# Optimization experiments

Measured on AMD Instinct MI355X. Metric: run time of the kernel, lower is better.

## Reference

```python
import jax, jax.numpy as jnp
import numpy as np

N_NODES = 100000
IN_C, HID_C, OUT_C = 128, 64, 5
NEG_SLOPE = 0.01  # F.leaky_relu default


def gcn_conv(x, W, b, src_sl, dst_sl, norm, n_nodes):
    """PyG GCNConv: h = D^{-1/2}(A+I)D^{-1/2} (x W) + b.
    src_sl/dst_sl already include self-loops; norm is the per-edge coefficient."""
    h = x @ W                              # [N, out]
    msg = h[src_sl] * norm[:, None]        # [E+N, out] gather + scale
    agg = jax.ops.segment_sum(msg, dst_sl, num_segments=n_nodes)
    return agg + b


def setup_inputs() -> dict:
    key = jax.random.key(0)
    ks = jax.random.split(key, 8)
    n, e = N_NODES, 1600000
    x = jax.random.normal(ks[0], (n, IN_C), dtype=jnp.float32)
    edge_index = jax.random.randint(ks[1], (2, e), 0, n, dtype=jnp.int64)
    idx = jax.random.randint(ks[2], (20000,), 0, n, dtype=jnp.int64)
    # Glorot-ish init for GCNConv weights, kaiming-ish for MLP
    W0 = jax.random.normal(ks[3], (IN_C, HID_C), dtype=jnp.float32) * (1.0 / np.sqrt(IN_C))
    b0 = jnp.zeros((HID_C,), dtype=jnp.float32)
    W1 = jax.random.normal(ks[4], (HID_C, HID_C), dtype=jnp.float32) * (1.0 / np.sqrt(HID_C))
    b1 = jnp.zeros((HID_C,), dtype=jnp.float32)
    Wm = jax.random.normal(ks[5], (HID_C, OUT_C), dtype=jnp.float32) * (1.0 / np.sqrt(HID_C))
    bm = jnp.zeros((OUT_C,), dtype=jnp.float32)
    return {"x": x, "edge_index": edge_index, "idx": idx,
            "W0": W0, "b0": b0, "W1": W1, "b1": b1, "Wm": Wm, "bm": bm}


def reference(x, edge_index, idx, W0, b0, W1, b1, Wm, bm):
    n = x.shape[0]
    src, dst = edge_index[0], edge_index[1]
    loops = jnp.arange(n, dtype=edge_index.dtype)
    src_sl = jnp.concatenate([src, loops])
    dst_sl = jnp.concatenate([dst, loops])
    # symmetric normalization with self-loops (gcn_norm)
    deg = jax.ops.segment_sum(jnp.ones_like(dst_sl, dtype=x.dtype), dst_sl, num_segments=n)
    dinv = jnp.where(deg > 0, jax.lax.rsqrt(deg), 0.0)
    norm = dinv[src_sl] * dinv[dst_sl]     # [E+N]

    h = jax.nn.leaky_relu(gcn_conv(x, W0, b0, src_sl, dst_sl, norm, n), NEG_SLOPE)
    h = jax.nn.leaky_relu(gcn_conv(h, W1, b1, src_sl, dst_sl, norm, n), NEG_SLOPE)

    h_sel = h[idx]                          # index_select on node dim
    out = jax.nn.sigmoid(h_sel @ Wm + bm)
    return (h_sel, out)
```

## Files before the change

### kernel.cpp

```cpp
#include <hip/hip_runtime.h>
#include <hip/hip_fp16.h>
#include <math.h>


#define NPART 256
#define MAXB 2048

typedef _Float16 h8 __attribute__((ext_vector_type(8)));
typedef float f4v __attribute__((ext_vector_type(4)));

__device__ __forceinline__ float lrelu(float x) { return x > 0.0f ? x : 0.01f * x; }


__global__ __launch_bounds__(1024) void k_part_hist(const int* __restrict__ dst, int E,
                                                    int B, int* __restrict__ phist) {
    __shared__ int scnt[MAXB];
    int t = threadIdx.x, p = blockIdx.x;
    for (int i = t; i < B; i += 1024) scnt[i] = 0;
    __syncthreads();
    int ep = (((E + NPART - 1) / NPART) + 3) & ~3;
    int beg = p * ep, endi = min(E, beg + ep);
    int cnt4 = (endi - beg) >> 2;
    for (int i = t; i < cnt4; i += 1024) {
        int4 d = *(const int4*)(dst + beg + i * 4);
        atomicAdd(&scnt[d.x >> 6], 1);
        atomicAdd(&scnt[d.y >> 6], 1);
        atomicAdd(&scnt[d.z >> 6], 1);
        atomicAdd(&scnt[d.w >> 6], 1);
    }
    int rem = (endi - beg) & 3;
    if (t < rem) atomicAdd(&scnt[dst[beg + cnt4 * 4 + t] >> 6], 1);
    __syncthreads();
    for (int i = t; i < B; i += 1024) phist[i * NPART + p] = scnt[i];
}

__global__ __launch_bounds__(1024) void k_part_scatter(const int* __restrict__ src,
                                                       const int* __restrict__ dst, int E,
                                                       int B, const int* __restrict__ pbase,
                                                       int* __restrict__ esA) {
    __shared__ int sbase[MAXB];
    int t = threadIdx.x, p = blockIdx.x;
    for (int i = t; i < B; i += 1024) sbase[i] = pbase[i * NPART + p];
    __syncthreads();
    int ep = (((E + NPART - 1) / NPART) + 3) & ~3;
    int beg = p * ep, endi = min(E, beg + ep);
    int cnt4 = (endi - beg) >> 2;
    for (int i = t; i < cnt4; i += 1024) {
        int e = beg + i * 4;
        int4 d = *(const int4*)(dst + e);
        int4 s = *(const int4*)(src + e);
        int p0 = atomicAdd(&sbase[d.x >> 6], 1);
        int p1 = atomicAdd(&sbase[d.y >> 6], 1);
        int p2 = atomicAdd(&sbase[d.z >> 6], 1);
        int p3 = atomicAdd(&sbase[d.w >> 6], 1);
        esA[p0] = ((d.x & 63) << 24) | s.x;
        esA[p1] = ((d.y & 63) << 24) | s.y;
        esA[p2] = ((d.z & 63) << 24) | s.z;
        esA[p3] = ((d.w & 63) << 24) | s.w;
    }
    int rem = (endi - beg) & 3;
    if (t < rem) {
        int e = beg + cnt4 * 4 + t;
        int d = dst[e];
        int pos = atomicAdd(&sbase[d >> 6], 1);
        esA[pos] = ((d & 63) << 24) | src[e];
    }
}


__global__ void k_blocksum(const int* __restrict__ cnt, int N, int* __restrict__ bsum) {
    __shared__ int sm[256];
    int b = blockIdx.x, t = threadIdx.x;
    int base = b * 1024 + t * 4;
    int s = 0;
#pragma unroll
    for (int i = 0; i < 4; ++i) { int j = base + i; if (j < N) s += cnt[j]; }
    sm[t] = s; __syncthreads();
    for (int off = 128; off > 0; off >>= 1) {
        if (t < off) sm[t] += sm[t + off];
        __syncthreads();
    }
    if (t == 0) bsum[b] = sm[0];
}

__global__ void k_scan_bsum(int* __restrict__ bsum, int nb, int* __restrict__ offN) {
    __shared__ int sm[1024];
    int t = threadIdx.x;
    int v = (t < nb) ? bsum[t] : 0;
    sm[t] = v; __syncthreads();
    for (int d = 1; d < 1024; d <<= 1) {
        int add = (t >= d) ? sm[t - d] : 0;
        __syncthreads();
        sm[t] += add;
        __syncthreads();
    }
    if (t < nb) bsum[t] = sm[t] - v;
    if (t == nb - 1) *offN = sm[t];
}

__global__ void k_scan_block(const int* __restrict__ cnt, const int* __restrict__ bsum,
                             int* __restrict__ off, int N) {
    __shared__ int sm[256];
    int b = blockIdx.x, t = threadIdx.x;
    int base = b * 1024 + t * 4;
    int v[4];
#pragma unroll
    for (int i = 0; i < 4; ++i) { int j = base + i; v[i] = (j < N) ? cnt[j] : 0; }
    int tsum = v[0] + v[1] + v[2] + v[3];
    sm[t] = tsum; __syncthreads();
    for (int d = 1; d < 256; d <<= 1) {
        int val = (t >= d) ? sm[t - d] : 0;
        __syncthreads();
        sm[t] += val;
        __syncthreads();
    }
    int run = sm[t] - tsum + bsum[b];
#pragma unroll
    for (int i = 0; i < 4; ++i) {
        int j = base + i;
        if (j < N) off[j] = run;
        run += v[i];
    }
}


__global__ __launch_bounds__(256) void k_bsort(const int* __restrict__ pbase, int BP,
                                               const int* __restrict__ esA,
                                               int* __restrict__ esB,
                                               int* __restrict__ off,
                                               float* __restrict__ dinv,
                                               int N, int E) {
    __shared__ int hcnt[64];
    __shared__ int hoff[64];
    int t = threadIdx.x, b = blockIdx.x;
    int start = pbase[b * NPART];
    int endi  = pbase[min((b + 1) * NPART, BP)];
    int cnt = endi - start;

    if (t < 64) hcnt[t] = 0;
    __syncthreads();
    for (int i = t * 4; i < cnt; i += 1024) {
#pragma unroll
        for (int c = 0; c < 4; ++c)
            if (i + c < cnt) atomicAdd(&hcnt[(esA[start + i + c] >> 24) & 63], 1);
    }
    __syncthreads();

    if (t < 64) {
        int c = hcnt[t];
        int v = c;
#pragma unroll
        for (int d = 1; d < 64; d <<= 1) {
            int u = __shfl_up(v, d);
            if (t >= d) v += u;
        }
        int pos = start + (v - c);
        hoff[t] = pos;
        int g = b * 64 + t;
        if (g < N) {
            off[g] = pos;
            dinv[g] = rsqrtf((float)c + 1.0f);
        }
        if (g == N - 1) off[N] = E;
    }
    __syncthreads();
    if (t < 64) hcnt[t] = hoff[t];
    __syncthreads();

    for (int i = t * 4; i < cnt; i += 1024) {
#pragma unroll
        for (int c = 0; c < 4; ++c)
            if (i + c < cnt) {
                int v = esA[start + i + c];
                int pos = atomicAdd(&hcnt[(v >> 24) & 63], 1);
                esB[pos] = v & 0xFFFFFF;
            }
    }
}


template <int K, typename AT>
__global__ __launch_bounds__(256) void k_gemm(const AT* __restrict__ A,
                                              const float* __restrict__ W,
                                              const float* __restrict__ dinv,
                                              __half* __restrict__ hout, int N) {
    constexpr int ASTR = K + 8;
    __shared__ _Float16 a16[64 * ASTR];
    __shared__ _Float16 wt16[64 * ASTR];
    int t = threadIdx.x, lane = t & 63, wv = t >> 6;
    int rowBase = blockIdx.x * 64;

#pragma unroll
    for (int i = 0; i < K / 16; ++i) {
        int g = i * 256 + t;
        int r = g / (K / 4), kq = g % (K / 4);
        int gr = rowBase + r; if (gr >= N) gr = N - 1;
        _Float16* p = a16 + r * ASTR + kq * 4;
        if constexpr (sizeof(AT) == 4) {
            float4 v = *(const float4*)((const float*)A + (size_t)gr * K + kq * 4);
            *(__half2*)(p)     = __floats2half2_rn(v.x, v.y);
            *(__half2*)(p + 2) = __floats2half2_rn(v.z, v.w);
        } else {
            *(uint2*)p = *(const uint2*)((const __half*)A + (size_t)gr * K + kq * 4);
        }
    }
#pragma unroll
    for (int i = 0; i < K / 16; ++i) {
        int g = i * 256 + t;
        int k = g >> 4, nq = g & 15;
        float4 v = *(const float4*)(W + (size_t)k * 64 + nq * 4);
        wt16[(nq * 4 + 0) * ASTR + k] = (_Float16)v.x;
        wt16[(nq * 4 + 1) * ASTR + k] = (_Float16)v.y;
        wt16[(nq * 4 + 2) * ASTR + k] = (_Float16)v.z;
        wt16[(nq * 4 + 3) * ASTR + k] = (_Float16)v.w;
    }
    __syncthreads();

    int m = lane & 15, q = lane >> 4;
    f4v acc[4] = {{0,0,0,0},{0,0,0,0},{0,0,0,0},{0,0,0,0}};
    const _Float16* arow = a16 + (wv * 16 + m) * ASTR + q * 8;
#pragma unroll
    for (int kt = 0; kt < K / 32; ++kt) {
        h8 af = *(const h8*)(arow + kt * 32);
#pragma unroll
        for (int nt = 0; nt < 4; ++nt) {
            h8 bf = *(const h8*)(wt16 + (nt * 16 + m) * ASTR + kt * 32 + q * 8);
            acc[nt] = __builtin_amdgcn_mfma_f32_16x16x32_f16(af, bf, acc[nt], 0, 0, 0);
        }
    }

    int r0 = rowBase + wv * 16 + q * 4;
#pragma unroll
    for (int reg = 0; reg < 4; ++reg) {
        int row = r0 + reg;
        if (row >= N) continue;
        float dv = dinv[row];
#pragma unroll
        for (int nt = 0; nt < 4; ++nt)
            hout[(size_t)row * 64 + nt * 16 + m] = (__half)(acc[nt][reg] * dv);
    }
}


__global__ __launch_bounds__(256) void k_agg1(const int* __restrict__ off,
                                              const int* __restrict__ esB,
                                              const float* __restrict__ dinv,
                                              const __half* __restrict__ hs,
                                              const float* __restrict__ b0,
                                              __half* __restrict__ aout, int N) {
    int lane = threadIdx.x & 63;
    int node = (blockIdx.x * blockDim.x + threadIdx.x) >> 6;
    if (node >= N) return;
    int qt = lane >> 4, l16 = lane & 15;
    int beg = off[node], end = off[node + 1];
    float dv = dinv[node];
    float4 b = *(const float4*)(b0 + l16 * 4);

    float ax = 0, ay = 0, az = 0, aw = 0;
    auto ld = [&](int s) { return *(const uint2*)(hs + (size_t)s * 64 + l16 * 4); };
    auto acc4 = [&](uint2 u) {
        float2 f0 = __half22float2(*(__half2*)&u.x);
        float2 f1 = __half22float2(*(__half2*)&u.y);
        ax += f0.x; ay += f0.y; az += f1.x; aw += f1.y;
    };
    if (qt == 0) acc4(ld(node));

    for (int base = beg; base < end; base += 64) {
        int nb = min(end - base, 64);
        int myIdx = esB[min(base + lane, end - 1)];
        if (nb <= 16) {
            int s0 = __shfl(myIdx, min(qt,      nb - 1));
            int s1 = __shfl(myIdx, min(qt + 4,  nb - 1));
            int s2 = __shfl(myIdx, min(qt + 8,  nb - 1));
            int s3 = __shfl(myIdx, min(qt + 12, nb - 1));
            uint2 u0 = ld(s0), u1 = ld(s1), u2 = ld(s2), u3 = ld(s3);
            if (qt      < nb) acc4(u0);
            if (qt + 4  < nb) acc4(u1);
            if (qt + 8  < nb) acc4(u2);
            if (qt + 12 < nb) acc4(u3);
        } else {
            int s0 = __shfl(myIdx, min(qt,      nb - 1));
            int s1 = __shfl(myIdx, min(qt + 4,  nb - 1));
            int s2 = __shfl(myIdx, min(qt + 8,  nb - 1));
            int s3 = __shfl(myIdx, min(qt + 12, nb - 1));
            int s4 = __shfl(myIdx, min(qt + 16, nb - 1));
            int s5 = __shfl(myIdx, min(qt + 20, nb - 1));
            int s6 = __shfl(myIdx, min(qt + 24, nb - 1));
            int s7 = __shfl(myIdx, min(qt + 28, nb - 1));
            uint2 u0 = ld(s0), u1 = ld(s1), u2 = ld(s2), u3 = ld(s3);
            uint2 u4 = ld(s4), u5 = ld(s5), u6 = ld(s6), u7 = ld(s7);
            acc4(u0);
            if (qt + 4  < nb) acc4(u1);
            if (qt + 8  < nb) acc4(u2);
            if (qt + 12 < nb) acc4(u3);
            if (qt + 16 < nb) acc4(u4);
            if (qt + 20 < nb) acc4(u5);
            if (qt + 24 < nb) acc4(u6);
            if (qt + 28 < nb) acc4(u7);
            if (nb > 32) {
                int t0 = __shfl(myIdx, min(qt + 32, nb - 1));
                int t1 = __shfl(myIdx, min(qt + 36, nb - 1));
                int t2 = __shfl(myIdx, min(qt + 40, nb - 1));
                int t3 = __shfl(myIdx, min(qt + 44, nb - 1));
                int t4 = __shfl(myIdx, min(qt + 48, nb - 1));
                int t5 = __shfl(myIdx, min(qt + 52, nb - 1));
                int t6 = __shfl(myIdx, min(qt + 56, nb - 1));
                int t7 = __shfl(myIdx, min(qt + 60, nb - 1));
                uint2 v0 = ld(t0), v1 = ld(t1), v2 = ld(t2), v3 = ld(t3);
                uint2 v4 = ld(t4), v5 = ld(t5), v6 = ld(t6), v7 = ld(t7);
                if (qt + 32 < nb) acc4(v0);
                if (qt + 36 < nb) acc4(v1);
                if (qt + 40 < nb) acc4(v2);
                if (qt + 44 < nb) acc4(v3);
                if (qt + 48 < nb) acc4(v4);
                if (qt + 52 < nb) acc4(v5);
                if (qt + 56 < nb) acc4(v6);
                if (qt + 60 < nb) acc4(v7);
            }
        }
    }

#pragma unroll
    for (int d = 16; d <= 32; d <<= 1) {
        ax += __shfl_xor(ax, d); ay += __shfl_xor(ay, d);
        az += __shfl_xor(az, d); aw += __shfl_xor(aw, d);
    }
    if (qt == 0) {
        float ox = lrelu(ax * dv + b.x), oy = lrelu(ay * dv + b.y);
        float oz = lrelu(az * dv + b.z), ow = lrelu(aw * dv + b.w);
        uint2 u;
        *(__half2*)&u.x = __floats2half2_rn(ox, oy);
        *(__half2*)&u.y = __floats2half2_rn(oz, ow);
        *(uint2*)(aout + (size_t)node * 64 + l16 * 4) = u;
    }
}


__global__ __launch_bounds__(256) void k_aggout(const int* __restrict__ idx,
                                                const int* __restrict__ off,
                                                const int* __restrict__ esB,
                                                const float* __restrict__ dinv,
                                                const __half* __restrict__ hs,
                                                const float* __restrict__ b1,
                                                const float* __restrict__ Wm,
                                                const float* __restrict__ bm,
                                                float* __restrict__ out, int NSEL) {
    int lane = threadIdx.x & 63;
    int wv = (blockIdx.x * blockDim.x + threadIdx.x) >> 6;
    if (wv >= NSEL) return;
    int node = idx[wv];
    int qt = lane >> 4, l16 = lane & 15;
    int beg = off[node], end = off[node + 1];
    float dv = dinv[node];
    float4 b = *(const float4*)(b1 + l16 * 4);

    float ax = 0, ay = 0, az = 0, aw = 0;
    auto ld = [&](int s) { return *(const uint2*)(hs + (size_t)s * 64 + l16 * 4); };
    auto acc4 = [&](uint2 u) {
        float2 f0 = __half22float2(*(__half2*)&u.x);
        float2 f1 = __half22float2(*(__half2*)&u.y);
        ax += f0.x; ay += f0.y; az += f1.x; aw += f1.y;
    };
    if (qt == 0) acc4(ld(node));

    for (int base = beg; base < end; base += 64) {
        int nb = min(end - base, 64);
        int myIdx = esB[min(base + lane, end - 1)];
        if (nb <= 16) {
            int s0 = __shfl(myIdx, min(qt,      nb - 1));
            int s1 = __shfl(myIdx, min(qt + 4,  nb - 1));
            int s2 = __shfl(myIdx, min(qt + 8,  nb - 1));
            int s3 = __shfl(myIdx, min(qt + 12, nb - 1));
            uint2 u0 = ld(s0), u1 = ld(s1), u2 = ld(s2), u3 = ld(s3);
            if (qt      < nb) acc4(u0);
            if (qt + 4  < nb) acc4(u1);
            if (qt + 8  < nb) acc4(u2);
            if (qt + 12 < nb) acc4(u3);
        } else {
            int s0 = __shfl(myIdx, min(qt,      nb - 1));
            int s1 = __shfl(myIdx, min(qt + 4,  nb - 1));
            int s2 = __shfl(myIdx, min(qt + 8,  nb - 1));
            int s3 = __shfl(myIdx, min(qt + 12, nb - 1));
            int s4 = __shfl(myIdx, min(qt + 16, nb - 1));
            int s5 = __shfl(myIdx, min(qt + 20, nb - 1));
            int s6 = __shfl(myIdx, min(qt + 24, nb - 1));
            int s7 = __shfl(myIdx, min(qt + 28, nb - 1));
            uint2 u0 = ld(s0), u1 = ld(s1), u2 = ld(s2), u3 = ld(s3);
            uint2 u4 = ld(s4), u5 = ld(s5), u6 = ld(s6), u7 = ld(s7);
            acc4(u0);
            if (qt + 4  < nb) acc4(u1);
            if (qt + 8  < nb) acc4(u2);
            if (qt + 12 < nb) acc4(u3);
            if (qt + 16 < nb) acc4(u4);
            if (qt + 20 < nb) acc4(u5);
            if (qt + 24 < nb) acc4(u6);
            if (qt + 28 < nb) acc4(u7);
            if (nb > 32) {
                int t0 = __shfl(myIdx, min(qt + 32, nb - 1));
                int t1 = __shfl(myIdx, min(qt + 36, nb - 1));
                int t2 = __shfl(myIdx, min(qt + 40, nb - 1));
                int t3 = __shfl(myIdx, min(qt + 44, nb - 1));
                int t4 = __shfl(myIdx, min(qt + 48, nb - 1));
                int t5 = __shfl(myIdx, min(qt + 52, nb - 1));
                int t6 = __shfl(myIdx, min(qt + 56, nb - 1));
                int t7 = __shfl(myIdx, min(qt + 60, nb - 1));
                uint2 v0 = ld(t0), v1 = ld(t1), v2 = ld(t2), v3 = ld(t3);
                uint2 v4 = ld(t4), v5 = ld(t5), v6 = ld(t6), v7 = ld(t7);
                if (qt + 32 < nb) acc4(v0);
                if (qt + 36 < nb) acc4(v1);
                if (qt + 40 < nb) acc4(v2);
                if (qt + 44 < nb) acc4(v3);
                if (qt + 48 < nb) acc4(v4);
                if (qt + 52 < nb) acc4(v5);
                if (qt + 56 < nb) acc4(v6);
                if (qt + 60 < nb) acc4(v7);
            }
        }
    }

#pragma unroll
    for (int d = 16; d <= 32; d <<= 1) {
        ax += __shfl_xor(ax, d); ay += __shfl_xor(ay, d);
        az += __shfl_xor(az, d); aw += __shfl_xor(aw, d);
    }

    float4 hsel;
    hsel.x = lrelu(ax * dv + b.x); hsel.y = lrelu(ay * dv + b.y);
    hsel.z = lrelu(az * dv + b.z); hsel.w = lrelu(aw * dv + b.w);
    if (qt == 0) *(float4*)(out + (size_t)wv * 64 + l16 * 4) = hsel;

    const float* wr = Wm + (size_t)(4 * l16) * 5;
#pragma unroll
    for (int o = 0; o < 5; ++o) {
        float p = hsel.x * wr[o] + hsel.y * wr[5 + o] +
                  hsel.z * wr[10 + o] + hsel.w * wr[15 + o];
        p += __shfl_xor(p, 1); p += __shfl_xor(p, 2);
        p += __shfl_xor(p, 4); p += __shfl_xor(p, 8);
        if (lane == 0)
            out[(size_t)NSEL * 64 + (size_t)wv * 5 + o] =
                1.0f / (1.0f + expf(-(p + bm[o])));
    }
}

extern "C" void kernel_launch(void* const* d_in, const int* in_sizes, int n_in,
                              void* d_out, int out_size, void* d_ws, size_t ws_size,
                              hipStream_t stream) {
    const float* x   = (const float*)d_in[0];
    const int*   ei  = (const int*)d_in[1];
    const int*   idx = (const int*)d_in[2];
    const float* W0  = (const float*)d_in[3];
    const float* b0  = (const float*)d_in[4];
    const float* W1  = (const float*)d_in[5];
    const float* b1  = (const float*)d_in[6];
    const float* Wm  = (const float*)d_in[7];
    const float* bm  = (const float*)d_in[8];

    int N    = in_sizes[0] / 128;
    int E    = in_sizes[1] / 2;
    int NSEL = in_sizes[2];
    const int* src = ei;
    const int* dst = ei + E;

    int B  = (N + 63) / 64;
    int BP = B * NPART;

    char* w = (char*)d_ws;
    size_t Na  = ((size_t)N + 1023) & ~(size_t)1023;
    size_t Ea  = ((size_t)E + 1023) & ~(size_t)1023;
    size_t BPa = ((size_t)BP + 1023) & ~(size_t)1023;
    float*  dinv  = (float*)w;                w += Na * 4;
    int*    phist = (int*)w;                  w += BPa * 4;
    int*    pbase = (int*)w;                  w += (BPa + 1024) * 4;
    int*    bsum  = (int*)w;                  w += 1024 * 4;
    int*    off   = (int*)w;                  w += (Na + 1024) * 4;
    int*    esA   = (int*)w;                  w += Ea * 4;
    int*    esB   = (int*)w;                  w += Ea * 4;
    __half* hs16  = (__half*)w;               w += (size_t)N * 64 * 2;
    __half* a16g  = (__half*)w;

    int nbp = (BP + 1023) / 1024;

    k_part_hist<<<NPART, 1024, 0, stream>>>(dst, E, B, phist);
    k_blocksum<<<nbp, 256, 0, stream>>>(phist, BP, bsum);
    k_scan_bsum<<<1, 1024, 0, stream>>>(bsum, nbp, pbase + BP);
    k_scan_block<<<nbp, 256, 0, stream>>>(phist, bsum, pbase, BP);
    k_part_scatter<<<NPART, 1024, 0, stream>>>(src, dst, E, B, pbase, esA);
    k_bsort<<<B, 256, 0, stream>>>(pbase, BP, esA, esB, off, dinv, N, E);

    int gemm_blocks = (N + 63) / 64;
    int agg_blocks  = (N + 3) / 4;

    k_gemm<128, float><<<gemm_blocks, 256, 0, stream>>>(x, W0, dinv, hs16, N);
    k_agg1<<<agg_blocks, 256, 0, stream>>>(off, esB, dinv, hs16, b0, a16g, N);
    k_gemm<64, __half><<<gemm_blocks, 256, 0, stream>>>(a16g, W1, dinv, hs16, N);
    k_aggout<<<(NSEL + 3) / 4, 256, 0, stream>>>(idx, off, esB, dinv, hs16, b1, Wm, bm,
                                                 (float*)d_out, NSEL);
}
```

Baseline: 242.5 us.

## Replace two-level partitioned CSR build with global-atomic counting sort

Replaces the two-pass LDS-partitioned bucket sort (partition histogram, partition scatter, per-bucket sort) with a direct build: global atomic degree count, a prefix scan over nodes that also writes the dinv normalization, and a scatter that uses global atomic cursors. This removes a kernel launch and an extra pass over the intermediate edge array, and it shrinks the scan from N/64*256 entries to N. In exchange it relies on contended global atomics over 100k counters, scatters edges randomly to global memory, and leaves edge order within each row nondeterministic.

```diff
diff --git a/kernel.cpp b/kernel.cpp
--- a/kernel.cpp
+++ b/kernel.cpp
@@ -3,68 +3,25 @@
 #include <math.h>
 
 
-#define NPART 256
-#define MAXB 2048
-
 typedef _Float16 h8 __attribute__((ext_vector_type(8)));
 typedef float f4v __attribute__((ext_vector_type(4)));
 
 __device__ __forceinline__ float lrelu(float x) { return x > 0.0f ? x : 0.01f * x; }
 
 
-__global__ __launch_bounds__(1024) void k_part_hist(const int* __restrict__ dst, int E,
-                                                    int B, int* __restrict__ phist) {
-    __shared__ int scnt[MAXB];
-    int t = threadIdx.x, p = blockIdx.x;
-    for (int i = t; i < B; i += 1024) scnt[i] = 0;
-    __syncthreads();
-    int ep = (((E + NPART - 1) / NPART) + 3) & ~3;
-    int beg = p * ep, endi = min(E, beg + ep);
-    int cnt4 = (endi - beg) >> 2;
-    for (int i = t; i < cnt4; i += 1024) {
-        int4 d = *(const int4*)(dst + beg + i * 4);
-        atomicAdd(&scnt[d.x >> 6], 1);
-        atomicAdd(&scnt[d.y >> 6], 1);
-        atomicAdd(&scnt[d.z >> 6], 1);
-        atomicAdd(&scnt[d.w >> 6], 1);
-    }
-    int rem = (endi - beg) & 3;
-    if (t < rem) atomicAdd(&scnt[dst[beg + cnt4 * 4 + t] >> 6], 1);
-    __syncthreads();
-    for (int i = t; i < B; i += 1024) phist[i * NPART + p] = scnt[i];
-}
-
-__global__ __launch_bounds__(1024) void k_part_scatter(const int* __restrict__ src,
-                                                       const int* __restrict__ dst, int E,
-                                                       int B, const int* __restrict__ pbase,
-                                                       int* __restrict__ esA) {
-    __shared__ int sbase[MAXB];
-    int t = threadIdx.x, p = blockIdx.x;
-    for (int i = t; i < B; i += 1024) sbase[i] = pbase[i * NPART + p];
-    __syncthreads();
-    int ep = (((E + NPART - 1) / NPART) + 3) & ~3;
-    int beg = p * ep, endi = min(E, beg + ep);
-    int cnt4 = (endi - beg) >> 2;
-    for (int i = t; i < cnt4; i += 1024) {
-        int e = beg + i * 4;
-        int4 d = *(const int4*)(dst + e);
-        int4 s = *(const int4*)(src + e);
-        int p0 = atomicAdd(&sbase[d.x >> 6], 1);
-        int p1 = atomicAdd(&sbase[d.y >> 6], 1);
-        int p2 = atomicAdd(&sbase[d.z >> 6], 1);
-        int p3 = atomicAdd(&sbase[d.w >> 6], 1);
-        esA[p0] = ((d.x & 63) << 24) | s.x;
-        esA[p1] = ((d.y & 63) << 24) | s.y;
-        esA[p2] = ((d.z & 63) << 24) | s.z;
-        esA[p3] = ((d.w & 63) << 24) | s.w;
-    }
-    int rem = (endi - beg) & 3;
-    if (t < rem) {
-        int e = beg + cnt4 * 4 + t;
-        int d = dst[e];
-        int pos = atomicAdd(&sbase[d >> 6], 1);
-        esA[pos] = ((d & 63) << 24) | src[e];
-    }
+__global__ __launch_bounds__(256) void k_deg(const int* __restrict__ dst, int E,
+                                             int* __restrict__ deg) {
+    int tid = blockIdx.x * blockDim.x + threadIdx.x;
+    int stride = gridDim.x * blockDim.x;
+    int cnt4 = E >> 2;
+    for (int i = tid; i < cnt4; i += stride) {
+        int4 d = *(const int4*)(dst + i * 4);
+        atomicAdd(&deg[d.x], 1);
+        atomicAdd(&deg[d.y], 1);
+        atomicAdd(&deg[d.z], 1);
+        atomicAdd(&deg[d.w], 1);
+    }
+    if (tid < (E & 3)) atomicAdd(&deg[dst[cnt4 * 4 + tid]], 1);
 }
 
 
@@ -99,7 +56,8 @@
 }
 
 __global__ void k_scan_block(const int* __restrict__ cnt, const int* __restrict__ bsum,
-                             int* __restrict__ off, int N) {
+                             int* __restrict__ off, int* __restrict__ cur,
+                             float* __restrict__ dinv, int N) {
     __shared__ int sm[256];
     int b = blockIdx.x, t = threadIdx.x;
     int base = b * 1024 + t * 4;
@@ -118,63 +76,40 @@
 #pragma unroll
     for (int i = 0; i < 4; ++i) {
         int j = base + i;
-        if (j < N) off[j] = run;
+        if (j < N) {
+            off[j] = run;
+            cur[j] = run;
+            dinv[j] = rsqrtf((float)v[i] + 1.0f);
+        }
         run += v[i];
     }
 }
 
 
-__global__ __launch_bounds__(256) void k_bsort(const int* __restrict__ pbase, int BP,
-                                               const int* __restrict__ esA,
-                                               int* __restrict__ esB,
-                                               int* __restrict__ off,
-                                               float* __restrict__ dinv,
-                                               int N, int E) {
-    __shared__ int hcnt[64];
-    __shared__ int hoff[64];
-    int t = threadIdx.x, b = blockIdx.x;
-    int start = pbase[b * NPART];
-    int endi  = pbase[min((b + 1) * NPART, BP)];
-    int cnt = endi - start;
-
-    if (t < 64) hcnt[t] = 0;
-    __syncthreads();
-    for (int i = t * 4; i < cnt; i += 1024) {
-#pragma unroll
-        for (int c = 0; c < 4; ++c)
-            if (i + c < cnt) atomicAdd(&hcnt[(esA[start + i + c] >> 24) & 63], 1);
-    }
-    __syncthreads();
-
-    if (t < 64) {
-        int c = hcnt[t];
-        int v = c;
-#pragma unroll
-        for (int d = 1; d < 64; d <<= 1) {
-            int u = __shfl_up(v, d);
-            if (t >= d) v += u;
-        }
-        int pos = start + (v - c);
-        hoff[t] = pos;
-        int g = b * 64 + t;
-        if (g < N) {
-            off[g] = pos;
-            dinv[g] = rsqrtf((float)c + 1.0f);
-        }
-        if (g == N - 1) off[N] = E;
-    }
-    __syncthreads();
-    if (t < 64) hcnt[t] = hoff[t];
-    __syncthreads();
-
-    for (int i = t * 4; i < cnt; i += 1024) {
-#pragma unroll
-        for (int c = 0; c < 4; ++c)
-            if (i + c < cnt) {
-                int v = esA[start + i + c];
-                int pos = atomicAdd(&hcnt[(v >> 24) & 63], 1);
-                esB[pos] = v & 0xFFFFFF;
-            }
+__global__ __launch_bounds__(256) void k_scatterd(const int* __restrict__ src,
+                                                  const int* __restrict__ dst, int E,
+                                                  int* __restrict__ cur,
+                                                  int* __restrict__ esB) {
+    int tid = blockIdx.x * blockDim.x + threadIdx.x;
+    int stride = gridDim.x * blockDim.x;
+    int cnt4 = E >> 2;
+    for (int i = tid; i < cnt4; i += stride) {
+        int e = i * 4;
+        int4 d = *(const int4*)(dst + e);
+        int4 s = *(const int4*)(src + e);
+        int p0 = atomicAdd(&cur[d.x], 1);
+        int p1 = atomicAdd(&cur[d.y], 1);
+        int p2 = atomicAdd(&cur[d.z], 1);
+        int p3 = atomicAdd(&cur[d.w], 1);
+        esB[p0] = s.x;
+        esB[p1] = s.y;
+        esB[p2] = s.z;
+        esB[p3] = s.w;
+    }
+    if (tid < (E & 3)) {
+        int e = cnt4 * 4 + tid;
+        int pos = atomicAdd(&cur[dst[e]], 1);
+        esB[pos] = src[e];
     }
 }
 
@@ -461,31 +396,28 @@
     const int* src = ei;
     const int* dst = ei + E;
 
-    int B  = (N + 63) / 64;
-    int BP = B * NPART;
-
     char* w = (char*)d_ws;
     size_t Na  = ((size_t)N + 1023) & ~(size_t)1023;
     size_t Ea  = ((size_t)E + 1023) & ~(size_t)1023;
-    size_t BPa = ((size_t)BP + 1023) & ~(size_t)1023;
     float*  dinv  = (float*)w;                w += Na * 4;
-    int*    phist = (int*)w;                  w += BPa * 4;
-    int*    pbase = (int*)w;                  w += (BPa + 1024) * 4;
+    int*    deg   = (int*)w;                  w += Na * 4;
+    int*    off   = (int*)w;                  w += (Na + 1024) * 4;
+    int*    cur   = (int*)w;                  w += Na * 4;
     int*    bsum  = (int*)w;                  w += 1024 * 4;
-    int*    off   = (int*)w;                  w += (Na + 1024) * 4;
-    int*    esA   = (int*)w;                  w += Ea * 4;
     int*    esB   = (int*)w;                  w += Ea * 4;
     __half* hs16  = (__half*)w;               w += (size_t)N * 64 * 2;
     __half* a16g  = (__half*)w;
 
-    int nbp = (BP + 1023) / 1024;
-
-    k_part_hist<<<NPART, 1024, 0, stream>>>(dst, E, B, phist);
-    k_blocksum<<<nbp, 256, 0, stream>>>(phist, BP, bsum);
-    k_scan_bsum<<<1, 1024, 0, stream>>>(bsum, nbp, pbase + BP);
-    k_scan_block<<<nbp, 256, 0, stream>>>(phist, bsum, pbase, BP);
-    k_part_scatter<<<NPART, 1024, 0, stream>>>(src, dst, E, B, pbase, esA);
-    k_bsort<<<B, 256, 0, stream>>>(pbase, BP, esA, esB, off, dinv, N, E);
+    int nbp = (N + 1023) / 1024;
+
+    hipMemsetAsync(deg, 0, (size_t)N * 4, stream);
+
+    int ek_blocks = min(2048, (E / 4 + 255) / 256);
+    k_deg<<<ek_blocks, 256, 0, stream>>>(dst, E, deg);
+    k_blocksum<<<nbp, 256, 0, stream>>>(deg, N, bsum);
+    k_scan_bsum<<<1, 1024, 0, stream>>>(bsum, nbp, off + N);
+    k_scan_block<<<nbp, 256, 0, stream>>>(deg, bsum, off, cur, dinv, N);
+    k_scatterd<<<ek_blocks, 256, 0, stream>>>(src, dst, E, cur, esB);
 
     int gemm_blocks = (N + 63) / 64;
     int agg_blocks  = (N + 3) / 4;
```

Result: slower. 406.9 us (+67.7%).
